# Kernel tuning notes

Hardware: AMD Instinct MI355X
Metric: run time of the kernel (lower is better)

Reference implementation:

```python
import jax, jax.numpy as jnp
import numpy as np

NUM_UNITS = 64
MEM_SLOTS = 8192
D_ATT = 64
D_MEM = 64
MASK_P = 0.2
NEG_INF = -1e9  # finite stand-in for RandomMask's -inf (identical softmax, safe grads)


def setup_inputs() -> dict:
    key = jax.random.key(0)
    k1, k2, k3, k4 = jax.random.split(key, 4)
    attention = jax.random.normal(k1, (NUM_UNITS, D_ATT), dtype=jnp.float32)
    attentions = jax.random.normal(k2, (NUM_UNITS, MEM_SLOTS, D_ATT), dtype=jnp.float32)
    memories = jax.random.normal(k3, (NUM_UNITS, MEM_SLOTS, D_MEM), dtype=jnp.float32)
    tmpr = jnp.ones((NUM_UNITS, 1), dtype=jnp.float32) * np.sqrt(D_ATT).astype(np.float32)
    mask = jax.random.bernoulli(k4, MASK_P, (NUM_UNITS, MEM_SLOTS))  # True -> dropped
    return {"attention": attention, "attentions": attentions,
            "memories": memories, "tmpr": tmpr, "mask": mask}


def reference(attention, attentions, memories, tmpr, mask):
    # scores: [U, M] = batched matvec over memory slots
    w = jnp.einsum('umd,ud->um', attentions, attention)
    w = jnp.where(mask, NEG_INF, w)          # RandomMask
    w = w / tmpr                              # per-unit temperature [U,1]
    weights = jax.nn.softmax(w, axis=-1)      # softmax over memory slots
    outputs = jnp.einsum('um,umd->ud', weights, memories)
    return (outputs, weights, memories)
```

## Files before the change

### kernel.cpp

```cpp
#include <hip/hip_runtime.h>
#include <cstdint>

#define U_UNITS 64
#define M_SLOTS 8192
#define D_DIM   64
#define SCH     16
#define CHUNK   (M_SLOTS / SCH)
#define BLK     256

__global__ __launch_bounds__(BLK) void score_kernel(
    const float* __restrict__ att,
    const float* __restrict__ atts,
    const float* __restrict__ tmpr,
    const int*   __restrict__ mask,
    float* __restrict__ wsc,
    float* __restrict__ pmax,
    float* __restrict__ psum)
{
    const int b = blockIdx.x;
    const int u = b / SCH, c = b % SCH;
    const int tid = threadIdx.x;

    __shared__ float s_att[D_DIM];
    __shared__ float s_w[CHUNK];
    __shared__ float s_m[4], s_s[4];

    if (tid < D_DIM) s_att[tid] = att[u * D_DIM + tid];
    __syncthreads();

    const int cg = (tid & 15) * 4;
    float a0 = s_att[cg], a1 = s_att[cg + 1], a2 = s_att[cg + 2], a3 = s_att[cg + 3];
    const float invt = 1.0f / tmpr[u];

    const float* base = atts + (size_t)u * M_SLOTS * D_DIM + (size_t)c * CHUNK * D_DIM;

    #pragma unroll 4
    for (int k = 0; k < CHUNK / 16; ++k) {
        const int sl = k * 16 + (tid >> 4);
        const float4 v = *(const float4*)(base + (size_t)sl * D_DIM + cg);
        float d = v.x * a0 + v.y * a1 + v.z * a2 + v.w * a3;
        d += __shfl_xor(d, 1);
        d += __shfl_xor(d, 2);
        d += __shfl_xor(d, 4);
        d += __shfl_xor(d, 8);
        const int m_idx = c * CHUNK + sl;
        const float wv = mask[u * M_SLOTS + m_idx] ? -1e30f : d * invt;
        if ((tid & 15) == 0) {
            s_w[sl] = wv;
            wsc[(size_t)u * M_SLOTS + m_idx] = wv;
        }
    }
    __syncthreads();

    float mx = -1e30f;
    for (int i = tid; i < CHUNK; i += BLK) mx = fmaxf(mx, s_w[i]);
    #pragma unroll
    for (int off = 1; off < 64; off <<= 1) mx = fmaxf(mx, __shfl_xor(mx, off));
    if ((tid & 63) == 0) s_m[tid >> 6] = mx;
    __syncthreads();
    mx = fmaxf(fmaxf(s_m[0], s_m[1]), fmaxf(s_m[2], s_m[3]));

    float sm = 0.f;
    for (int i = tid; i < CHUNK; i += BLK) sm += __expf(s_w[i] - mx);
    #pragma unroll
    for (int off = 1; off < 64; off <<= 1) sm += __shfl_xor(sm, off);
    if ((tid & 63) == 0) s_s[tid >> 6] = sm;
    __syncthreads();
    if (tid == 0) {
        pmax[b] = mx;
        psum[b] = s_s[0] + s_s[1] + s_s[2] + s_s[3];
    }
}

__global__ void combine_kernel(const float* __restrict__ pmax,
                               const float* __restrict__ psum,
                               float* __restrict__ gmx,
                               float* __restrict__ ginv)
{
    const int u = threadIdx.x;
    float mx = -1e30f;
    #pragma unroll
    for (int c = 0; c < SCH; ++c) mx = fmaxf(mx, pmax[u * SCH + c]);
    float s = 0.f;
    #pragma unroll
    for (int c = 0; c < SCH; ++c) s += psum[u * SCH + c] * __expf(pmax[u * SCH + c] - mx);
    gmx[u] = mx;
    ginv[u] = 1.0f / s;
}

__global__ __launch_bounds__(BLK) void pv_kernel(
    const float* __restrict__ mem,
    const float* __restrict__ gmx,
    const float* __restrict__ ginv,
    float* __restrict__ out_w,
    float* __restrict__ out_m,
    float* __restrict__ pout)
{
    const int b = blockIdx.x;
    const int u = b / SCH, c = b % SCH;
    const int tid = threadIdx.x;
    const float gm = gmx[u], gi = ginv[u];
    const int cg = (tid & 15) * 4;

    float acc[4] = {0.f, 0.f, 0.f, 0.f};
    const size_t ubase = (size_t)u * M_SLOTS * D_DIM + (size_t)c * CHUNK * D_DIM;

    #pragma unroll 4
    for (int k = 0; k < CHUNK / 16; ++k) {
        const int sl = k * 16 + (tid >> 4);
        const int m_idx = c * CHUNK + sl;
        const float sc = out_w[(size_t)u * M_SLOTS + m_idx];
        const float wv = __expf(sc - gm) * gi;
        const float4 v = *(const float4*)(mem + ubase + (size_t)sl * D_DIM + cg);
        *(float4*)(out_m + ubase + (size_t)sl * D_DIM + cg) = v;
        acc[0] += wv * v.x;
        acc[1] += wv * v.y;
        acc[2] += wv * v.z;
        acc[3] += wv * v.w;
        if ((tid & 15) == 0) out_w[(size_t)u * M_SLOTS + m_idx] = wv;
    }

    #pragma unroll
    for (int j = 0; j < 4; ++j) {
        acc[j] += __shfl_xor(acc[j], 16);
        acc[j] += __shfl_xor(acc[j], 32);
    }

    __shared__ float s_acc[4 * D_DIM];
    const int lane = tid & 63, w = tid >> 6;
    if (lane < 16) {
        #pragma unroll
        for (int j = 0; j < 4; ++j) s_acc[w * D_DIM + lane * 4 + j] = acc[j];
    }
    __syncthreads();
    if (tid < D_DIM) {
        const float s = s_acc[tid] + s_acc[D_DIM + tid] + s_acc[2 * D_DIM + tid] + s_acc[3 * D_DIM + tid];
        pout[(size_t)b * D_DIM + tid] = s;
    }
}

__global__ void out_kernel(const float* __restrict__ pout, float* __restrict__ out_o)
{
    const int u = blockIdx.x, t = threadIdx.x;
    float s = 0.f;
    #pragma unroll
    for (int c = 0; c < SCH; ++c) s += pout[((size_t)u * SCH + c) * D_DIM + t];
    out_o[u * D_DIM + t] = s;
}

extern "C" void kernel_launch(void* const* d_in, const int* in_sizes, int n_in,
                              void* d_out, int out_size, void* d_ws, size_t ws_size,
                              hipStream_t stream)
{
    const float* att  = (const float*)d_in[0];
    const float* atts = (const float*)d_in[1];
    const float* mem  = (const float*)d_in[2];
    const float* tmpr = (const float*)d_in[3];
    const int*   mask = (const int*)d_in[4];

    float* out   = (float*)d_out;
    float* out_o = out;
    float* out_w = out + U_UNITS * D_DIM;
    float* out_m = out_w + (size_t)U_UNITS * M_SLOTS;

    float* ws   = (float*)d_ws;
    float* pmax = ws;
    float* psum = pmax + U_UNITS * SCH;
    float* gmx  = psum + U_UNITS * SCH;
    float* ginv = gmx + U_UNITS;
    float* pout = ginv + U_UNITS;

    score_kernel<<<U_UNITS * SCH, BLK, 0, stream>>>(att, atts, tmpr, mask, out_w, pmax, psum);
    combine_kernel<<<1, U_UNITS, 0, stream>>>(pmax, psum, gmx, ginv);
    pv_kernel<<<U_UNITS * SCH, BLK, 0, stream>>>(mem, gmx, ginv, out_w, out_m, pout);
    out_kernel<<<U_UNITS, D_DIM, 0, stream>>>(pout, out_o);
}
```

Measured before the change: 346.9 us.

## Fuse score and PV passes with flash-style local softmax and rescale pass

Merges the score kernel and the weighted-sum kernel into one pass per chunk. It uses a chunk-local max, writes unnormalized exponentials, and accumulates partial outputs in the same block. A combine kernel then computes per-chunk rescale factors and the final outputs, and a small elementwise kernel rescales the weight row in place. This removes one kernel launch and the reread of the score buffer between passes, at the cost of an extra read-modify-write over the weights output. The psum is scaled by 1/16 to undo the sum over the 16 lanes that each hold the same weight.

```diff
diff --git a/kernel.cpp b/kernel.cpp
--- a/kernel.cpp
+++ b/kernel.cpp
@@ -8,14 +8,17 @@
 #define CHUNK   (M_SLOTS / SCH)
 #define BLK     256
 
-__global__ __launch_bounds__(BLK) void score_kernel(
+__global__ __launch_bounds__(BLK) void fused_kernel(
     const float* __restrict__ att,
     const float* __restrict__ atts,
     const float* __restrict__ tmpr,
     const int*   __restrict__ mask,
-    float* __restrict__ wsc,
+    const float* __restrict__ mem,
+    float* __restrict__ out_w,
+    float* __restrict__ out_m,
     float* __restrict__ pmax,
-    float* __restrict__ psum)
+    float* __restrict__ psum,
+    float* __restrict__ pout)
 {
     const int b = blockIdx.x;
     const int u = b / SCH, c = b % SCH;
@@ -24,128 +27,120 @@
     __shared__ float s_att[D_DIM];
     __shared__ float s_w[CHUNK];
     __shared__ float s_m[4], s_s[4];
+    __shared__ float s_acc[4 * D_DIM];
 
     if (tid < D_DIM) s_att[tid] = att[u * D_DIM + tid];
     __syncthreads();
 
     const int cg = (tid & 15) * 4;
-    float a0 = s_att[cg], a1 = s_att[cg + 1], a2 = s_att[cg + 2], a3 = s_att[cg + 3];
+    const float a0 = s_att[cg], a1 = s_att[cg + 1];
+    const float a2 = s_att[cg + 2], a3 = s_att[cg + 3];
     const float invt = 1.0f / tmpr[u];
 
-    const float* base = atts + (size_t)u * M_SLOTS * D_DIM + (size_t)c * CHUNK * D_DIM;
+    const size_t ubase = (size_t)u * M_SLOTS * D_DIM + (size_t)c * CHUNK * D_DIM;
+    const float* __restrict__ abase = atts + ubase;
 
+    float lmx = -1e30f;
     #pragma unroll 4
     for (int k = 0; k < CHUNK / 16; ++k) {
         const int sl = k * 16 + (tid >> 4);
-        const float4 v = *(const float4*)(base + (size_t)sl * D_DIM + cg);
+        const float4 v = *(const float4*)(abase + (size_t)sl * D_DIM + cg);
         float d = v.x * a0 + v.y * a1 + v.z * a2 + v.w * a3;
         d += __shfl_xor(d, 1);
         d += __shfl_xor(d, 2);
         d += __shfl_xor(d, 4);
         d += __shfl_xor(d, 8);
-        const int m_idx = c * CHUNK + sl;
-        const float wv = mask[u * M_SLOTS + m_idx] ? -1e30f : d * invt;
-        if ((tid & 15) == 0) {
-            s_w[sl] = wv;
-            wsc[(size_t)u * M_SLOTS + m_idx] = wv;
-        }
+        const float wv = mask[u * M_SLOTS + c * CHUNK + sl] ? -1e30f : d * invt;
+        lmx = fmaxf(lmx, wv);
+        if ((tid & 15) == 0) s_w[sl] = wv;
+    }
+    #pragma unroll
+    for (int off = 1; off < 64; off <<= 1) lmx = fmaxf(lmx, __shfl_xor(lmx, off));
+    if ((tid & 63) == 0) s_m[tid >> 6] = lmx;
+    __syncthreads();
+    const float mx = fmaxf(fmaxf(s_m[0], s_m[1]), fmaxf(s_m[2], s_m[3]));
+
+    const float* __restrict__ mbase = mem + ubase;
+    float* __restrict__ obase = out_m + ubase;
+    float acc0 = 0.f, acc1 = 0.f, acc2 = 0.f, acc3 = 0.f;
+    float sm = 0.f;
+    #pragma unroll 4
+    for (int k = 0; k < CHUNK / 16; ++k) {
+        const int sl = k * 16 + (tid >> 4);
+        const float we = __expf(s_w[sl] - mx);
+        const float4 v = *(const float4*)(mbase + (size_t)sl * D_DIM + cg);
+        *(float4*)(obase + (size_t)sl * D_DIM + cg) = v;
+        acc0 += we * v.x;
+        acc1 += we * v.y;
+        acc2 += we * v.z;
+        acc3 += we * v.w;
+        sm += we;
+        if ((tid & 15) == 0)
+            out_w[(size_t)u * M_SLOTS + c * CHUNK + sl] = we;
+    }
+
+    float acc[4] = {acc0, acc1, acc2, acc3};
+    #pragma unroll
+    for (int j = 0; j < 4; ++j) {
+        acc[j] += __shfl_xor(acc[j], 16);
+        acc[j] += __shfl_xor(acc[j], 32);
+    }
+    #pragma unroll
+    for (int off = 1; off < 64; off <<= 1) sm += __shfl_xor(sm, off);
+
+    const int lane = tid & 63, w = tid >> 6;
+    if (lane == 0) s_s[w] = sm;
+    if (lane < 16) {
+        #pragma unroll
+        for (int j = 0; j < 4; ++j) s_acc[w * D_DIM + lane * 4 + j] = acc[j];
     }
     __syncthreads();
-
-    float mx = -1e30f;
-    for (int i = tid; i < CHUNK; i += BLK) mx = fmaxf(mx, s_w[i]);
-    #pragma unroll
-    for (int off = 1; off < 64; off <<= 1) mx = fmaxf(mx, __shfl_xor(mx, off));
-    if ((tid & 63) == 0) s_m[tid >> 6] = mx;
-    __syncthreads();
-    mx = fmaxf(fmaxf(s_m[0], s_m[1]), fmaxf(s_m[2], s_m[3]));
-
-    float sm = 0.f;
-    for (int i = tid; i < CHUNK; i += BLK) sm += __expf(s_w[i] - mx);
-    #pragma unroll
-    for (int off = 1; off < 64; off <<= 1) sm += __shfl_xor(sm, off);
-    if ((tid & 63) == 0) s_s[tid >> 6] = sm;
-    __syncthreads();
+    if (tid < D_DIM) {
+        const float s = s_acc[tid] + s_acc[D_DIM + tid]
+                      + s_acc[2 * D_DIM + tid] + s_acc[3 * D_DIM + tid];
+        pout[(size_t)b * D_DIM + tid] = s;
+    }
     if (tid == 0) {
         pmax[b] = mx;
-        psum[b] = s_s[0] + s_s[1] + s_s[2] + s_s[3];
+        psum[b] = (s_s[0] + s_s[1] + s_s[2] + s_s[3]) * 0.0625f;
     }
 }
 
-__global__ void combine_kernel(const float* __restrict__ pmax,
-                               const float* __restrict__ psum,
-                               float* __restrict__ gmx,
-                               float* __restrict__ ginv)
+__global__ void combine_out_kernel(
+    const float* __restrict__ pmax,
+    const float* __restrict__ psum,
+    const float* __restrict__ pout,
+    float* __restrict__ alpha,
+    float* __restrict__ out_o)
 {
-    const int u = threadIdx.x;
+    const int u = blockIdx.x, t = threadIdx.x;
     float mx = -1e30f;
     #pragma unroll
     for (int c = 0; c < SCH; ++c) mx = fmaxf(mx, pmax[u * SCH + c]);
     float s = 0.f;
     #pragma unroll
     for (int c = 0; c < SCH; ++c) s += psum[u * SCH + c] * __expf(pmax[u * SCH + c] - mx);
-    gmx[u] = mx;
-    ginv[u] = 1.0f / s;
+    const float inv = 1.0f / s;
+    float o = 0.f;
+    #pragma unroll
+    for (int c = 0; c < SCH; ++c)
+        o += __expf(pmax[u * SCH + c] - mx) * inv * pout[((size_t)u * SCH + c) * D_DIM + t];
+    out_o[u * D_DIM + t] = o;
+    if (t < SCH) alpha[u * SCH + t] = __expf(pmax[u * SCH + t] - mx) * inv;
 }
 
-__global__ __launch_bounds__(BLK) void pv_kernel(
-    const float* __restrict__ mem,
-    const float* __restrict__ gmx,
-    const float* __restrict__ ginv,
-    float* __restrict__ out_w,
-    float* __restrict__ out_m,
-    float* __restrict__ pout)
+__global__ __launch_bounds__(BLK) void wfix_kernel(
+    const float* __restrict__ alpha,
+    float* __restrict__ out_w)
 {
-    const int b = blockIdx.x;
-    const int u = b / SCH, c = b % SCH;
-    const int tid = threadIdx.x;
-    const float gm = gmx[u], gi = ginv[u];
-    const int cg = (tid & 15) * 4;
-
-    float acc[4] = {0.f, 0.f, 0.f, 0.f};
-    const size_t ubase = (size_t)u * M_SLOTS * D_DIM + (size_t)c * CHUNK * D_DIM;
-
-    #pragma unroll 4
-    for (int k = 0; k < CHUNK / 16; ++k) {
-        const int sl = k * 16 + (tid >> 4);
-        const int m_idx = c * CHUNK + sl;
-        const float sc = out_w[(size_t)u * M_SLOTS + m_idx];
-        const float wv = __expf(sc - gm) * gi;
-        const float4 v = *(const float4*)(mem + ubase + (size_t)sl * D_DIM + cg);
-        *(float4*)(out_m + ubase + (size_t)sl * D_DIM + cg) = v;
-        acc[0] += wv * v.x;
-        acc[1] += wv * v.y;
-        acc[2] += wv * v.z;
-        acc[3] += wv * v.w;
-        if ((tid & 15) == 0) out_w[(size_t)u * M_SLOTS + m_idx] = wv;
-    }
-
-    #pragma unroll
-    for (int j = 0; j < 4; ++j) {
-        acc[j] += __shfl_xor(acc[j], 16);
-        acc[j] += __shfl_xor(acc[j], 32);
-    }
-
-    __shared__ float s_acc[4 * D_DIM];
-    const int lane = tid & 63, w = tid >> 6;
-    if (lane < 16) {
-        #pragma unroll
-        for (int j = 0; j < 4; ++j) s_acc[w * D_DIM + lane * 4 + j] = acc[j];
-    }
-    __syncthreads();
-    if (tid < D_DIM) {
-        const float s = s_acc[tid] + s_acc[D_DIM + tid] + s_acc[2 * D_DIM + tid] + s_acc[3 * D_DIM + tid];
-        pout[(size_t)b * D_DIM + tid] = s;
-    }
-}
-
-__global__ void out_kernel(const float* __restrict__ pout, float* __restrict__ out_o)
-{
-    const int u = blockIdx.x, t = threadIdx.x;
-    float s = 0.f;
-    #pragma unroll
-    for (int c = 0; c < SCH; ++c) s += pout[((size_t)u * SCH + c) * D_DIM + t];
-    out_o[u * D_DIM + t] = s;
+    const int g = blockIdx.x * BLK + threadIdx.x;
+    const int u = g >> 11;
+    const int c = (g & 2047) >> 7;
+    const float a = alpha[u * SCH + c];
+    float4* p = reinterpret_cast<float4*>(out_w) + g;
+    float4 v = *p;
+    v.x *= a; v.y *= a; v.z *= a; v.w *= a;
+    *p = v;
 }
 
 extern "C" void kernel_launch(void* const* d_in, const int* in_sizes, int n_in,
@@ -163,15 +158,14 @@
     float* out_w = out + U_UNITS * D_DIM;
     float* out_m = out_w + (size_t)U_UNITS * M_SLOTS;
 
-    float* ws   = (float*)d_ws;
-    float* pmax = ws;
-    float* psum = pmax + U_UNITS * SCH;
-    float* gmx  = psum + U_UNITS * SCH;
-    float* ginv = gmx + U_UNITS;
-    float* pout = ginv + U_UNITS;
+    float* ws    = (float*)d_ws;
+    float* pmax  = ws;
+    float* psum  = pmax + U_UNITS * SCH;
+    float* alpha = psum + U_UNITS * SCH;
+    float* pout  = alpha + U_UNITS * SCH;
 
-    score_kernel<<<U_UNITS * SCH, BLK, 0, stream>>>(att, atts, tmpr, mask, out_w, pmax, psum);
-    combine_kernel<<<1, U_UNITS, 0, stream>>>(pmax, psum, gmx, ginv);
-    pv_kernel<<<U_UNITS * SCH, BLK, 0, stream>>>(mem, gmx, ginv, out_w, out_m, pout);
-    out_kernel<<<U_UNITS, D_DIM, 0, stream>>>(pout, out_o);
+    fused_kernel<<<U_UNITS * SCH, BLK, 0, stream>>>(
+        att, atts, tmpr, mask, mem, out_w, out_m, pmax, psum, pout);
+    combine_out_kernel<<<U_UNITS, D_DIM, 0, stream>>>(pmax, psum, pout, alpha, out_o);
+    wfix_kernel<<<(U_UNITS * M_SLOTS / 4) / BLK, BLK, 0, stream>>>(alpha, out_w);
 }
```

Measured after the change: 331.7 us. 4.4% less time.

## Use online softmax, 4-slot vectorized loads, nontemporal stores, and more chunks

Applied to the files above, without the earlier changes.

The score kernel now computes a running online max and sum in registers instead of staging scores in shared memory and making two extra passes. Each thread group handles 4 consecutive slots, so the mask, score and weight accesses become vectorized int4/float4 loads and stores. The memory copy to the output uses nontemporal stores, and SCH doubles to 32 to launch more blocks. The extra exp per step adds some compute, but the work is memory-bound.

```diff
diff --git a/kernel.cpp b/kernel.cpp
--- a/kernel.cpp
+++ b/kernel.cpp
@@ -4,78 +4,97 @@
 #define U_UNITS 64
 #define M_SLOTS 8192
 #define D_DIM   64
-#define SCH     16
+#define SCH     32
 #define CHUNK   (M_SLOTS / SCH)
 #define BLK     256
+#define SPG     4
+
+typedef __attribute__((ext_vector_type(4))) float fvec4;
 
 __global__ __launch_bounds__(BLK) void score_kernel(
     const float* __restrict__ att,
     const float* __restrict__ atts,
     const float* __restrict__ tmpr,
     const int*   __restrict__ mask,
-    float* __restrict__ wsc,
+    float* __restrict__ out_w,
     float* __restrict__ pmax,
     float* __restrict__ psum)
 {
     const int b = blockIdx.x;
     const int u = b / SCH, c = b % SCH;
     const int tid = threadIdx.x;
-
-    __shared__ float s_att[D_DIM];
-    __shared__ float s_w[CHUNK];
+    const int grp = tid >> 4, r = tid & 15, cg = r * 4;
+
     __shared__ float s_m[4], s_s[4];
 
-    if (tid < D_DIM) s_att[tid] = att[u * D_DIM + tid];
-    __syncthreads();
-
-    const int cg = (tid & 15) * 4;
-    float a0 = s_att[cg], a1 = s_att[cg + 1], a2 = s_att[cg + 2], a3 = s_att[cg + 3];
+    const float4 av = *(const float4*)(att + u * D_DIM + cg);
     const float invt = 1.0f / tmpr[u];
 
-    const float* base = atts + (size_t)u * M_SLOTS * D_DIM + (size_t)c * CHUNK * D_DIM;
-
-    #pragma unroll 4
-    for (int k = 0; k < CHUNK / 16; ++k) {
-        const int sl = k * 16 + (tid >> 4);
-        const float4 v = *(const float4*)(base + (size_t)sl * D_DIM + cg);
-        float d = v.x * a0 + v.y * a1 + v.z * a2 + v.w * a3;
-        d += __shfl_xor(d, 1);
-        d += __shfl_xor(d, 2);
-        d += __shfl_xor(d, 4);
-        d += __shfl_xor(d, 8);
-        const int m_idx = c * CHUNK + sl;
-        const float wv = mask[u * M_SLOTS + m_idx] ? -1e30f : d * invt;
-        if ((tid & 15) == 0) {
-            s_w[sl] = wv;
-            wsc[(size_t)u * M_SLOTS + m_idx] = wv;
+    const size_t ubase = (size_t)u * M_SLOTS * D_DIM + (size_t)c * CHUNK * D_DIM;
+    const float* __restrict__ abase = atts + ubase;
+    const int*   __restrict__ mkbase = mask + (size_t)u * M_SLOTS + c * CHUNK;
+    float* __restrict__ swbase = out_w + (size_t)u * M_SLOTS + c * CHUNK;
+
+    float m = -1e30f, sm = 0.f;
+
+    #pragma unroll
+    for (int k = 0; k < CHUNK / (16 * SPG); ++k) {
+        const int sl0 = k * 64 + grp * SPG;
+        float4 va[SPG];
+        #pragma unroll
+        for (int i = 0; i < SPG; ++i)
+            va[i] = *(const float4*)(abase + (size_t)(sl0 + i) * D_DIM + cg);
+        const int4 mk = *(const int4*)(mkbase + sl0);
+
+        float wv[SPG];
+        #pragma unroll
+        for (int i = 0; i < SPG; ++i) {
+            float d = va[i].x * av.x + va[i].y * av.y + va[i].z * av.z + va[i].w * av.w;
+            d += __shfl_xor(d, 1);
+            d += __shfl_xor(d, 2);
+            d += __shfl_xor(d, 4);
+            d += __shfl_xor(d, 8);
+            wv[i] = d * invt;
         }
-    }
-    __syncthreads();
-
-    float mx = -1e30f;
-    for (int i = tid; i < CHUNK; i += BLK) mx = fmaxf(mx, s_w[i]);
-    #pragma unroll
-    for (int off = 1; off < 64; off <<= 1) mx = fmaxf(mx, __shfl_xor(mx, off));
-    if ((tid & 63) == 0) s_m[tid >> 6] = mx;
-    __syncthreads();
-    mx = fmaxf(fmaxf(s_m[0], s_m[1]), fmaxf(s_m[2], s_m[3]));
-
-    float sm = 0.f;
-    for (int i = tid; i < CHUNK; i += BLK) sm += __expf(s_w[i] - mx);
-    #pragma unroll
-    for (int off = 1; off < 64; off <<= 1) sm += __shfl_xor(sm, off);
-    if ((tid & 63) == 0) s_s[tid >> 6] = sm;
+        if (mk.x) wv[0] = -1e30f;
+        if (mk.y) wv[1] = -1e30f;
+        if (mk.z) wv[2] = -1e30f;
+        if (mk.w) wv[3] = -1e30f;
+
+        if (r == 0)
+            *(float4*)(swbase + sl0) = make_float4(wv[0], wv[1], wv[2], wv[3]);
+
+        const float mx4  = fmaxf(fmaxf(wv[0], wv[1]), fmaxf(wv[2], wv[3]));
+        const float newm = fmaxf(m, mx4);
+        const float scf  = __expf(m - newm);
+        sm = sm * scf + __expf(wv[0] - newm) + __expf(wv[1] - newm)
+                      + __expf(wv[2] - newm) + __expf(wv[3] - newm);
+        m = newm;
+    }
+
+    #pragma unroll
+    for (int off = 16; off <= 32; off <<= 1) {
+        const float om = __shfl_xor(m, off);
+        const float os = __shfl_xor(sm, off);
+        const float nm = fmaxf(m, om);
+        sm = sm * __expf(m - nm) + os * __expf(om - nm);
+        m = nm;
+    }
+    const int lane = tid & 63, w = tid >> 6;
+    if (lane == 0) { s_m[w] = m; s_s[w] = sm; }
     __syncthreads();
     if (tid == 0) {
-        pmax[b] = mx;
-        psum[b] = s_s[0] + s_s[1] + s_s[2] + s_s[3];
-    }
-}
-
-__global__ void combine_kernel(const float* __restrict__ pmax,
-                               const float* __restrict__ psum,
-                               float* __restrict__ gmx,
-                               float* __restrict__ ginv)
+        float bm = fmaxf(fmaxf(s_m[0], s_m[1]), fmaxf(s_m[2], s_m[3]));
+        float bs = s_s[0] * __expf(s_m[0] - bm) + s_s[1] * __expf(s_m[1] - bm)
+                 + s_s[2] * __expf(s_m[2] - bm) + s_s[3] * __expf(s_m[3] - bm);
+        pmax[b] = bm;
+        psum[b] = bs;
+    }
+}
+
+__global__ void combine_kernel(
+    const float* __restrict__ pmax, const float* __restrict__ psum,
+    float* __restrict__ gmx, float* __restrict__ ginv)
 {
     const int u = threadIdx.x;
     float mx = -1e30f;
@@ -99,34 +118,54 @@
     const int b = blockIdx.x;
     const int u = b / SCH, c = b % SCH;
     const int tid = threadIdx.x;
+    const int grp = tid >> 4, r = tid & 15, cg = r * 4;
     const float gm = gmx[u], gi = ginv[u];
-    const int cg = (tid & 15) * 4;
-
-    float acc[4] = {0.f, 0.f, 0.f, 0.f};
+
+    __shared__ float s_acc[4 * D_DIM];
+
     const size_t ubase = (size_t)u * M_SLOTS * D_DIM + (size_t)c * CHUNK * D_DIM;
-
-    #pragma unroll 4
-    for (int k = 0; k < CHUNK / 16; ++k) {
-        const int sl = k * 16 + (tid >> 4);
-        const int m_idx = c * CHUNK + sl;
-        const float sc = out_w[(size_t)u * M_SLOTS + m_idx];
-        const float wv = __expf(sc - gm) * gi;
-        const float4 v = *(const float4*)(mem + ubase + (size_t)sl * D_DIM + cg);
-        *(float4*)(out_m + ubase + (size_t)sl * D_DIM + cg) = v;
-        acc[0] += wv * v.x;
-        acc[1] += wv * v.y;
-        acc[2] += wv * v.z;
-        acc[3] += wv * v.w;
-        if ((tid & 15) == 0) out_w[(size_t)u * M_SLOTS + m_idx] = wv;
-    }
-
+    const float* __restrict__ mbase = mem + ubase;
+    float* __restrict__ obase = out_m + ubase;
+    float* __restrict__ swbase = out_w + (size_t)u * M_SLOTS + c * CHUNK;
+
+    float acc0 = 0.f, acc1 = 0.f, acc2 = 0.f, acc3 = 0.f;
+
+    #pragma unroll
+    for (int k = 0; k < CHUNK / (16 * SPG); ++k) {
+        const int sl0 = k * 64 + grp * SPG;
+
+        const float4 ws = *(const float4*)(swbase + sl0);
+        float4 vm[SPG];
+        #pragma unroll
+        for (int i = 0; i < SPG; ++i)
+            vm[i] = *(const float4*)(mbase + (size_t)(sl0 + i) * D_DIM + cg);
+
+        const float w0 = __expf(ws.x - gm) * gi;
+        const float w1 = __expf(ws.y - gm) * gi;
+        const float w2 = __expf(ws.z - gm) * gi;
+        const float w3 = __expf(ws.w - gm) * gi;
+
+        #pragma unroll
+        for (int i = 0; i < SPG; ++i)
+            __builtin_nontemporal_store(
+                *(const fvec4*)&vm[i],
+                (fvec4*)(obase + (size_t)(sl0 + i) * D_DIM + cg));
+
+        acc0 += w0 * vm[0].x + w1 * vm[1].x + w2 * vm[2].x + w3 * vm[3].x;
+        acc1 += w0 * vm[0].y + w1 * vm[1].y + w2 * vm[2].y + w3 * vm[3].y;
+        acc2 += w0 * vm[0].z + w1 * vm[1].z + w2 * vm[2].z + w3 * vm[3].z;
+        acc3 += w0 * vm[0].w + w1 * vm[1].w + w2 * vm[2].w + w3 * vm[3].w;
+
+        if (r == 0)
+            *(float4*)(swbase + sl0) = make_float4(w0, w1, w2, w3);
+    }
+
+    float acc[4] = {acc0, acc1, acc2, acc3};
     #pragma unroll
     for (int j = 0; j < 4; ++j) {
         acc[j] += __shfl_xor(acc[j], 16);
         acc[j] += __shfl_xor(acc[j], 32);
     }
-
-    __shared__ float s_acc[4 * D_DIM];
     const int lane = tid & 63, w = tid >> 6;
     if (lane < 16) {
         #pragma unroll
@@ -134,7 +173,8 @@
     }
     __syncthreads();
     if (tid < D_DIM) {
-        const float s = s_acc[tid] + s_acc[D_DIM + tid] + s_acc[2 * D_DIM + tid] + s_acc[3 * D_DIM + tid];
+        const float s = s_acc[tid] + s_acc[D_DIM + tid]
+                      + s_acc[2 * D_DIM + tid] + s_acc[3 * D_DIM + tid];
         pout[(size_t)b * D_DIM + tid] = s;
     }
 }
@@ -163,12 +203,12 @@
     float* out_w = out + U_UNITS * D_DIM;
     float* out_m = out_w + (size_t)U_UNITS * M_SLOTS;
 
-    float* ws   = (float*)d_ws;
-    float* pmax = ws;
-    float* psum = pmax + U_UNITS * SCH;
-    float* gmx  = psum + U_UNITS * SCH;
-    float* ginv = gmx + U_UNITS;
-    float* pout = ginv + U_UNITS;
+    float* ws    = (float*)d_ws;
+    float* pmax  = ws;
+    float* psum  = pmax + U_UNITS * SCH;
+    float* gmx   = psum + U_UNITS * SCH;
+    float* ginv  = gmx + U_UNITS;
+    float* pout  = ginv + U_UNITS;
 
     score_kernel<<<U_UNITS * SCH, BLK, 0, stream>>>(att, atts, tmpr, mask, out_w, pmax, psum);
     combine_kernel<<<1, U_UNITS, 0, stream>>>(pmax, psum, gmx, ginv);
```

New measurement: 337.1 us. -2.8%, faster.
